# Performance work log

Measured on AMD Instinct MI355X. Metric: run time of the kernel, lower is better.

## Reference

```python
import jax, jax.numpy as jnp
import numpy as np
from jax import lax

EPS = 1e-12  # F.normalize default eps


def setup_inputs() -> dict:
    key = jax.random.key(0)
    ks = jax.random.split(key, 4)
    b, dim, h, w = 8, 192, 128, 128
    num_heads = 6
    x = jax.random.normal(ks[0], (b, dim, h, w), dtype=jnp.float32)
    y = jax.random.normal(ks[1], (b, dim, h, w), dtype=jnp.float32)
    # depthwise conv weight (groups = 3*dim): [3*dim, 1, 3, 3]
    w_dw = jax.random.normal(ks[2], (3 * dim, 1, 3, 3), dtype=jnp.float32) * 0.1
    # 1x1 projection: [dim, dim]
    w_proj = jax.random.normal(ks[3], (dim, dim), dtype=jnp.float32) * (1.0 / np.sqrt(dim))
    temperature = jnp.ones((num_heads, 1, 1), dtype=jnp.float32)
    return {"x": x, "y": y, "w_dw": w_dw, "w_proj": w_proj,
            "temperature": temperature, "num_heads": num_heads}


def _l2norm(t):
    n = jnp.sqrt(jnp.sum(t * t, axis=-1, keepdims=True))
    return t / jnp.maximum(n, EPS)


def reference(x, y, w_dw, w_proj, temperature, num_heads):
    b, c, h, w = x.shape
    qkv_in = jnp.concatenate([x, y, y], axis=1)  # [b, 3c, h, w]
    # depthwise 3x3 conv, stride 1, padding 1 (groups = 3c)
    qkv = lax.conv_general_dilated(
        qkv_in, w_dw, window_strides=(1, 1), padding=((1, 1), (1, 1)),
        dimension_numbers=("NCHW", "OIHW", "NCHW"), feature_group_count=3 * c)
    q, k, v = jnp.split(qkv, 3, axis=1)
    ch = c // num_heads
    rs = lambda t: t.reshape(b, num_heads, ch, h * w)  # b head c (h w)
    q, k, v = rs(q), rs(k), rs(v)
    q = _l2norm(q)
    k = _l2norm(k)
    # channel attention: [b, head, ch, ch]
    attn = jnp.einsum("bhcn,bhdn->bhcd", q, k) * temperature
    attn = jax.nn.softmax(attn, axis=-1)
    out = jnp.einsum("bhcd,bhdn->bhcn", attn, v).reshape(b, c, h, w)
    # 1x1 conv projection
    out = jnp.einsum("oc,bchw->bohw", w_proj, out)
    return out
```

## Files before the change

### kernel.cpp

```cpp
#include <hip/hip_runtime.h>
#include <hip/hip_bf16.h>

#define DEV __device__ __forceinline__

typedef unsigned char u8;
typedef unsigned short u16;
typedef unsigned int u32;
typedef long long i64;
typedef __attribute__((ext_vector_type(8))) short short8;
typedef __attribute__((ext_vector_type(4))) float f32x4;

DEV u16 f2bf(float f) {
  __hip_bfloat16 h = __float2bfloat16(f);
  return *(u16*)&h;
}

#define NB 8
#define NH 6
#define CTOT 192
#define HW 16384
#define VTS 34
#define LSTR 136

__global__ __launch_bounds__(256) void kconv(
    const float* __restrict__ x, const float* __restrict__ y,
    const float* __restrict__ wdw,
    u8* __restrict__ qws, u8* __restrict__ kws, u16* __restrict__ vws,
    float* __restrict__ sqq, float* __restrict__ sqk)
{
  __shared__ __align__(16) float lds[34 * LSTR];
  const int t = threadIdx.x, lane = t & 63;
  const int bx   = blockIdx.x;
  const int iskv = bx & 1;
  const int rest = bx >> 1;
  const int qtr  = rest & 3;
  const int task = rest >> 2;
  const int b  = task / 192;
  const int gc = task % 192;
  const int r0 = qtr * 32;

  const float* __restrict__ in =
      (iskv ? y : x) + (((size_t)(b * CTOT + gc)) << 14);

  float w0[9], w1[9];
  if (!iskv) {
#pragma unroll
    for (int i = 0; i < 9; ++i) w0[i] = wdw[gc * 9 + i];
  } else {
#pragma unroll
    for (int i = 0; i < 9; ++i) {
      w0[i] = wdw[(CTOT + gc) * 9 + i];
      w1[i] = wdw[(2 * CTOT + gc) * 9 + i];
    }
  }

  if (t < 68) {
    const int row = t >> 1;
    lds[row * LSTR + ((t & 1) ? 132 : 3)] = 0.f;
  }
#pragma unroll
  for (int i = 0; i < 5; ++i) {
    const int idx = i * 256 + t;
    if (idx < 1088) {
      const int row = idx >> 5, c4 = idx & 31;
      const int grow = r0 - 1 + row;
      float4 v = (grow >= 0 && grow < 128)
          ? *(const float4*)(in + grow * 128 + c4 * 4)
          : make_float4(0.f, 0.f, 0.f, 0.f);
      *(float4*)&lds[row * LSTR + 4 + c4 * 4] = v;
    }
  }
  __syncthreads();

  const int j   = t & 31;
  const int seg = t >> 5;
  const int lr0 = seg * 4;

  u8*  __restrict__ out0 =
      (iskv ? kws : qws) + (((size_t)(b * CTOT + gc)) << 14);
  u16* __restrict__ out1 = vws + (((size_t)(b * CTOT + gc)) << 14);

  float R[6][6];
#pragma unroll
  for (int i = 0; i < 6; ++i) {
    const int base = (lr0 + i) * LSTR + 4 * j;
    const float4 a0 = *(const float4*)&lds[base];
    const float4 m  = *(const float4*)&lds[base + 4];
    const float4 a2 = *(const float4*)&lds[base + 8];
    R[i][0] = a0.w; R[i][1] = m.x; R[i][2] = m.y;
    R[i][3] = m.z;  R[i][4] = m.w; R[i][5] = a2.x;
  }

  float ssum = 0.f;

#pragma unroll
  for (int k = 0; k < 4; ++k) {
    const int r = r0 + lr0 + k;

    {
      float o0 = 0.f, o1 = 0.f, o2 = 0.f, o3 = 0.f;
#pragma unroll
      for (int dr = 0; dr < 3; ++dr) {
        const float* d = R[k + dr];
        o0 = fmaf(w0[dr * 3 + 0], d[0], o0); o0 = fmaf(w0[dr * 3 + 1], d[1], o0); o0 = fmaf(w0[dr * 3 + 2], d[2], o0);
        o1 = fmaf(w0[dr * 3 + 0], d[1], o1); o1 = fmaf(w0[dr * 3 + 1], d[2], o1); o1 = fmaf(w0[dr * 3 + 2], d[3], o1);
        o2 = fmaf(w0[dr * 3 + 0], d[2], o2); o2 = fmaf(w0[dr * 3 + 1], d[3], o2); o2 = fmaf(w0[dr * 3 + 2], d[4], o2);
        o3 = fmaf(w0[dr * 3 + 0], d[3], o3); o3 = fmaf(w0[dr * 3 + 1], d[4], o3); o3 = fmaf(w0[dr * 3 + 2], d[5], o3);
      }
      ssum = fmaf(o0, o0, ssum); ssum = fmaf(o1, o1, ssum);
      ssum = fmaf(o2, o2, ssum); ssum = fmaf(o3, o3, ssum);
      u32 p = (u32)__builtin_amdgcn_cvt_pk_fp8_f32(o0, o1, 0, false);
      p = (u32)__builtin_amdgcn_cvt_pk_fp8_f32(o2, o3, (int)p, true);
      *(u32*)(out0 + r * 128 + 4 * j) = p;
    }
    if (iskv) {
      float o0 = 0.f, o1 = 0.f, o2 = 0.f, o3 = 0.f;
#pragma unroll
      for (int dr = 0; dr < 3; ++dr) {
        const float* d = R[k + dr];
        o0 = fmaf(w1[dr * 3 + 0], d[0], o0); o0 = fmaf(w1[dr * 3 + 1], d[1], o0); o0 = fmaf(w1[dr * 3 + 2], d[2], o0);
        o1 = fmaf(w1[dr * 3 + 0], d[1], o1); o1 = fmaf(w1[dr * 3 + 1], d[2], o1); o1 = fmaf(w1[dr * 3 + 2], d[3], o1);
        o2 = fmaf(w1[dr * 3 + 0], d[2], o2); o2 = fmaf(w1[dr * 3 + 1], d[3], o2); o2 = fmaf(w1[dr * 3 + 2], d[4], o2);
        o3 = fmaf(w1[dr * 3 + 0], d[3], o3); o3 = fmaf(w1[dr * 3 + 1], d[4], o3); o3 = fmaf(w1[dr * 3 + 2], d[5], o3);
      }
      const u32 p01 = ((u32)f2bf(o1) << 16) | (u32)f2bf(o0);
      const u32 p23 = ((u32)f2bf(o3) << 16) | (u32)f2bf(o2);
      *(uint2*)(out1 + r * 128 + 4 * j) = make_uint2(p01, p23);
    }
  }

  ssum += __shfl_xor(ssum, 1);
  ssum += __shfl_xor(ssum, 2);
  ssum += __shfl_xor(ssum, 4);
  ssum += __shfl_xor(ssum, 8);
  ssum += __shfl_xor(ssum, 16);
  ssum += __shfl_xor(ssum, 32);
  if (lane == 0)
    atomicAdd((iskv ? sqk : sqq) + b * CTOT + gc, ssum);
}

__global__ __launch_bounds__(256) void k2a_gram(
    const u8* __restrict__ qws, const u8* __restrict__ kws,
    float* __restrict__ gram)
{
  const int t = threadIdx.x, l = t & 63, w = t >> 6;
  const int bh = blockIdx.x >> 4, tile = blockIdx.x & 15;
  const int p0 = tile * 1024 + w * 256;
  const u8* qb = qws + (((size_t)bh) << 19);
  const u8* kb = kws + (((size_t)bh) << 19);
  const int row = l & 15;
  const int kq  = (l >> 4) * 8;

  f32x4 acc[2][2] = {};

  for (int ks = 0; ks < 8; ++ks) {
    const int p = p0 + ks * 32 + kq;
    i64 av[2], bv[2];
#pragma unroll
    for (int tc = 0; tc < 2; ++tc) {
      av[tc] = *(const i64*)(qb + (((size_t)(tc * 16 + row)) << 14) + p);
      bv[tc] = *(const i64*)(kb + (((size_t)(tc * 16 + row)) << 14) + p);
    }
#pragma unroll
    for (int tc = 0; tc < 2; ++tc)
#pragma unroll
      for (int td = 0; td < 2; ++td)
        acc[tc][td] = __builtin_amdgcn_mfma_f32_16x16x32_fp8_fp8(av[tc], bv[td], acc[tc][td], 0, 0, 0);
  }

#pragma unroll
  for (int tc = 0; tc < 2; ++tc)
#pragma unroll
    for (int td = 0; td < 2; ++td)
#pragma unroll
      for (int rr = 0; rr < 4; ++rr) {
        int c = tc * 16 + (l >> 4) * 4 + rr;
        int d = td * 16 + row;
        atomicAdd(gram + (size_t)bh * 1024 + c * 32 + d, acc[tc][td][rr]);
      }
}

__global__ __launch_bounds__(256) void k2b_w2(
    const float* __restrict__ gram, const float* __restrict__ sqq,
    const float* __restrict__ sqk, const float* __restrict__ wp,
    const float* __restrict__ temp, u16* __restrict__ W2)
{
  __shared__ float Ls[32][33];
  __shared__ float As[32][33];
  __shared__ float wl[192 * 32];
  __shared__ float nq[32], nk[32];
  const int t = threadIdx.x;
  const int bh = blockIdx.x, b = bh / 6, h = bh % 6;
  const float tmp = temp[h];
  if (t < 32) nq[t] = fmaxf(sqrtf(sqq[b * CTOT + h * 32 + t]), 1e-12f);
  else if (t < 64) nk[t - 32] = fmaxf(sqrtf(sqk[b * CTOT + h * 32 + t - 32]), 1e-12f);
  __syncthreads();
#pragma unroll
  for (int i = 0; i < 4; ++i) {
    int idx = i * 256 + t, c = idx >> 5, d = idx & 31;
    Ls[c][d] = gram[(size_t)bh * 1024 + idx] / (nq[c] * nk[d]) * tmp;
  }
  __syncthreads();
  if (t < 32) {
    float m = -1e30f;
#pragma unroll
    for (int d = 0; d < 32; ++d) m = fmaxf(m, Ls[t][d]);
    float s = 0.f;
#pragma unroll
    for (int d = 0; d < 32; ++d) s += expf(Ls[t][d] - m);
    float inv = 1.0f / s;
#pragma unroll
    for (int d = 0; d < 32; ++d) As[t][d] = expf(Ls[t][d] - m) * inv;
  }
  for (int i = 0; i < 24; ++i) {
    int idx = i * 256 + t, o = idx >> 5, c = idx & 31;
    wl[idx] = wp[o * 192 + h * 32 + c];
  }
  __syncthreads();
  for (int i = 0; i < 24; ++i) {
    int idx = i * 256 + t, o = idx >> 5, d = idx & 31;
    float a = 0.f;
#pragma unroll
    for (int c = 0; c < 32; ++c) a = fmaf(wl[o * 32 + c], As[c][d], a);
    W2[((size_t)(b * 192 + o)) * 192 + h * 32 + d] = f2bf(a);
  }
}

__global__ __launch_bounds__(256) void k3_gemm(
    const u16* __restrict__ W2, const u16* __restrict__ vnat,
    float* __restrict__ out)
{
  __shared__ __align__(16) u16 b_tile[128 * VTS];
  __shared__ __align__(16) float cout[32 * 132];
  const int t = threadIdx.x, l = t & 63, w = t >> 6;
  const int bx = blockIdx.x;
  const int b  = bx >> 7, nb = bx & 127;
  const int arow = l & 15;
  const int kq8  = (l >> 4) * 8;
  const u16* w2b = W2 + (size_t)b * 192 * 192;
  const u16* vb  = vnat + ((size_t)b * CTOT) * HW;
  const int n0 = nb * 128;

  f32x4 acc[12][2] = {};

  for (int ks = 0; ks < 6; ++ks) {
    if (ks > 0) __syncthreads();
#pragma unroll
    for (int r2 = 0; r2 < 2; ++r2) {
      const int ch   = (t >> 4) + r2 * 16;
      const int nseg = (t & 15) * 8;
      short8 vv = *(const short8*)(vb + (size_t)(ks * 32 + ch) * HW + n0 + nseg);
#pragma unroll
      for (int j = 0; j < 8; ++j) b_tile[(nseg + j) * VTS + ch] = (u16)vv[j];
    }
    __syncthreads();

    short8 bf[2];
#pragma unroll
    for (int nt = 0; nt < 2; ++nt)
      bf[nt] = *(const short8*)&b_tile[(w * 32 + nt * 16 + arow) * VTS + kq8];
#pragma unroll
    for (int ot = 0; ot < 12; ++ot) {
      short8 af = *(const short8*)(w2b + (size_t)(ot * 16 + arow) * 192 + ks * 32 + kq8);
#pragma unroll
      for (int nt = 0; nt < 2; ++nt)
        acc[ot][nt] = __builtin_amdgcn_mfma_f32_16x16x32_bf16(af, bf[nt], acc[ot][nt], 0, 0, 0);
    }
  }

  float* __restrict__ ob = out + ((size_t)b * 192) * 16384;
#pragma unroll
  for (int og = 0; og < 6; ++og) {
    __syncthreads();
#pragma unroll
    for (int oi = 0; oi < 2; ++oi) {
#pragma unroll
      for (int nt = 0; nt < 2; ++nt)
#pragma unroll
        for (int rr = 0; rr < 4; ++rr) {
          const int o_l = oi * 16 + (l >> 4) * 4 + rr;
          const int n_l = w * 32 + nt * 16 + (l & 15);
          cout[o_l * 132 + n_l] = acc[og * 2 + oi][nt][rr];
        }
    }
    __syncthreads();
    const int o_l = t >> 3;
    const int o   = og * 32 + o_l;
#pragma unroll
    for (int c = 0; c < 4; ++c) {
      const int n = (t & 7) * 4 + c * 32;
      float4 v4;
      v4.x = cout[o_l * 132 + n + 0];
      v4.y = cout[o_l * 132 + n + 1];
      v4.z = cout[o_l * 132 + n + 2];
      v4.w = cout[o_l * 132 + n + 3];
      *(float4*)(ob + (size_t)o * 16384 + n0 + n) = v4;
    }
  }
}

extern "C" void kernel_launch(void* const* d_in, const int* in_sizes, int n_in,
                              void* d_out, int out_size, void* d_ws, size_t ws_size,
                              hipStream_t stream)
{
  const float* x    = (const float*)d_in[0];
  const float* y    = (const float*)d_in[1];
  const float* wdw  = (const float*)d_in[2];
  const float* wp   = (const float*)d_in[3];
  const float* temp = (const float*)d_in[4];

  char* ws = (char*)d_ws;
  const size_t QK8 = (size_t)NB * CTOT * HW;
  const size_t VBF = (size_t)NB * CTOT * HW * 2;
  u8*    qws  = (u8*)(ws);
  u8*    kws  = (u8*)(ws + QK8);
  u16*   vws  = (u16*)(ws + 2 * QK8);
  char*  meta = ws + 2 * QK8 + VBF;
  float* gram = (float*)(meta);
  float* sqq  = (float*)(meta + 196608);
  float* sqk  = (float*)(meta + 196608 + 6144);
  u16*   W2   = (u16*)(meta + 196608 + 12288);
  float* out  = (float*)d_out;

  hipMemsetAsync(meta, 0, 208896, stream);
  kconv<<<12288, 256, 0, stream>>>(x, y, wdw, qws, kws, vws, sqq, sqk);
  k2a_gram<<<768, 256, 0, stream>>>(qws, kws, gram);
  k2b_w2<<<48, 256, 0, stream>>>(gram, sqq, sqk, wp, temp, W2);
  k3_gemm<<<1024, 256, 0, stream>>>(W2, vws, out);
}
```

Before: 167.8 us.

## Double-buffer conv input via direct global-to-LDS loads, merge x/y blocks

Rewrites the depthwise conv kernel so each block handles half an image for both x and y channels, staging 16-row tiles into double-buffered LDS with global_load_lds while the previous tile is computed. Grid shrinks from 12288 to 3072 blocks, and the q, k and v convs plus both sum-of-squares reductions happen in one block. Out-of-range halo rows read from the zeroed gram buffer instead of branching, and column halos are handled by neighbour-index clamping. This aims to hide load latency and cut per-block overhead, at the cost of more LDS per block and reliance on the gram buffer being zero when kconv runs.

```diff
diff --git a/kernel.cpp b/kernel.cpp
--- a/kernel.cpp
+++ b/kernel.cpp
@@ -20,123 +20,135 @@
 #define CTOT 192
 #define HW 16384
 #define VTS 34
-#define LSTR 136
+#define SLAB 2304
+
+DEV void gload_lds(const float* src, float* dst) {
+  __builtin_amdgcn_global_load_lds(
+      (const __attribute__((address_space(1))) void*)src,
+      (__attribute__((address_space(3))) void*)dst, 16, 0, 0);
+}
 
 __global__ __launch_bounds__(256) void kconv(
     const float* __restrict__ x, const float* __restrict__ y,
-    const float* __restrict__ wdw,
+    const float* __restrict__ wdw, const float* __restrict__ zp,
     u8* __restrict__ qws, u8* __restrict__ kws, u16* __restrict__ vws,
     float* __restrict__ sqq, float* __restrict__ sqk)
 {
-  __shared__ __align__(16) float lds[34 * LSTR];
-  const int t = threadIdx.x, lane = t & 63;
+  __shared__ __align__(16) float bufX[2][SLAB];
+  __shared__ __align__(16) float bufY[2][SLAB];
+  const int t = threadIdx.x, lane = t & 63, w = t >> 6;
   const int bx   = blockIdx.x;
-  const int iskv = bx & 1;
-  const int rest = bx >> 1;
-  const int qtr  = rest & 3;
-  const int task = rest >> 2;
+  const int half = bx & 1;
+  const int task = bx >> 1;
   const int b  = task / 192;
   const int gc = task % 192;
-  const int r0 = qtr * 32;
-
-  const float* __restrict__ in =
-      (iskv ? y : x) + (((size_t)(b * CTOT + gc)) << 14);
-
-  float w0[9], w1[9];
-  if (!iskv) {
-#pragma unroll
-    for (int i = 0; i < 9; ++i) w0[i] = wdw[gc * 9 + i];
-  } else {
-#pragma unroll
-    for (int i = 0; i < 9; ++i) {
-      w0[i] = wdw[(CTOT + gc) * 9 + i];
-      w1[i] = wdw[(2 * CTOT + gc) * 9 + i];
-    }
-  }
-
-  if (t < 68) {
-    const int row = t >> 1;
-    lds[row * LSTR + ((t & 1) ? 132 : 3)] = 0.f;
-  }
-#pragma unroll
-  for (int i = 0; i < 5; ++i) {
-    const int idx = i * 256 + t;
-    if (idx < 1088) {
-      const int row = idx >> 5, c4 = idx & 31;
-      const int grow = r0 - 1 + row;
-      float4 v = (grow >= 0 && grow < 128)
-          ? *(const float4*)(in + grow * 128 + c4 * 4)
-          : make_float4(0.f, 0.f, 0.f, 0.f);
-      *(float4*)&lds[row * LSTR + 4 + c4 * 4] = v;
-    }
-  }
-  __syncthreads();
+  const int r0 = half * 64;
+
+  const float* __restrict__ inx = x + (((size_t)(b * CTOT + gc)) << 14);
+  const float* __restrict__ iny = y + (((size_t)(b * CTOT + gc)) << 14);
+
+  float wq[9], wk[9], wv[9];
+#pragma unroll
+  for (int i = 0; i < 9; ++i) {
+    wq[i] = wdw[gc * 9 + i];
+    wk[i] = wdw[(CTOT + gc) * 9 + i];
+    wv[i] = wdw[(2 * CTOT + gc) * 9 + i];
+  }
+
+  #define STAGE(bb, tt) { \
+      const int tr0s = r0 + (tt) * 16; \
+      const int px = (lane & 31) * 4; \
+      for (int l = w; l < 9; l += 4) { \
+        const int srow = tr0s - 1 + 2 * l + (lane >> 5); \
+        const bool ok = (srow >= 0) && (srow < 128); \
+        const float* sx = ok ? (inx + srow * 128 + px) : (zp + px); \
+        const float* sy = ok ? (iny + srow * 128 + px) : (zp + px); \
+        gload_lds(sx, &bufX[bb][l * 256]); \
+        gload_lds(sy, &bufY[bb][l * 256]); \
+      } }
 
   const int j   = t & 31;
   const int seg = t >> 5;
-  const int lr0 = seg * 4;
-
-  u8*  __restrict__ out0 =
-      (iskv ? kws : qws) + (((size_t)(b * CTOT + gc)) << 14);
-  u16* __restrict__ out1 = vws + (((size_t)(b * CTOT + gc)) << 14);
-
-  float R[6][6];
-#pragma unroll
-  for (int i = 0; i < 6; ++i) {
-    const int base = (lr0 + i) * LSTR + 4 * j;
-    const float4 a0 = *(const float4*)&lds[base];
-    const float4 m  = *(const float4*)&lds[base + 4];
-    const float4 a2 = *(const float4*)&lds[base + 8];
-    R[i][0] = a0.w; R[i][1] = m.x; R[i][2] = m.y;
-    R[i][3] = m.z;  R[i][4] = m.w; R[i][5] = a2.x;
-  }
-
-  float ssum = 0.f;
-
-#pragma unroll
-  for (int k = 0; k < 4; ++k) {
-    const int r = r0 + lr0 + k;
-
-    {
-      float o0 = 0.f, o1 = 0.f, o2 = 0.f, o3 = 0.f;
-#pragma unroll
-      for (int dr = 0; dr < 3; ++dr) {
-        const float* d = R[k + dr];
-        o0 = fmaf(w0[dr * 3 + 0], d[0], o0); o0 = fmaf(w0[dr * 3 + 1], d[1], o0); o0 = fmaf(w0[dr * 3 + 2], d[2], o0);
-        o1 = fmaf(w0[dr * 3 + 0], d[1], o1); o1 = fmaf(w0[dr * 3 + 1], d[2], o1); o1 = fmaf(w0[dr * 3 + 2], d[3], o1);
-        o2 = fmaf(w0[dr * 3 + 0], d[2], o2); o2 = fmaf(w0[dr * 3 + 1], d[3], o2); o2 = fmaf(w0[dr * 3 + 2], d[4], o2);
-        o3 = fmaf(w0[dr * 3 + 0], d[3], o3); o3 = fmaf(w0[dr * 3 + 1], d[4], o3); o3 = fmaf(w0[dr * 3 + 2], d[5], o3);
-      }
-      ssum = fmaf(o0, o0, ssum); ssum = fmaf(o1, o1, ssum);
-      ssum = fmaf(o2, o2, ssum); ssum = fmaf(o3, o3, ssum);
+
+  u8*  __restrict__ qout = qws + (((size_t)(b * CTOT + gc)) << 14);
+  u8*  __restrict__ kout = kws + (((size_t)(b * CTOT + gc)) << 14);
+  u16* __restrict__ vout = vws + (((size_t)(b * CTOT + gc)) << 14);
+
+  float ssq = 0.f, ssk = 0.f;
+
+  #define RDROW(buf, ri, d) { \
+      const float4 A = *(const float4*)&(buf)[(ri) * 128 + (j ? 4 * j - 4 : 0)]; \
+      const float4 M = *(const float4*)&(buf)[(ri) * 128 + 4 * j]; \
+      const float4 B = *(const float4*)&(buf)[(ri) * 128 + (j < 31 ? 4 * j + 4 : 124)]; \
+      d[0] = j ? A.w : 0.f; \
+      d[1] = M.x; d[2] = M.y; d[3] = M.z; d[4] = M.w; \
+      d[5] = (j < 31) ? B.x : 0.f; }
+
+  #define CONV4(Rw, wgt, k0, o0, o1, o2, o3) { \
+      o0 = o1 = o2 = o3 = 0.f; \
+      _Pragma("unroll") \
+      for (int dr = 0; dr < 3; ++dr) { \
+        const float* d = Rw[(k0) + dr]; \
+        o0 = fmaf(wgt[dr * 3 + 0], d[0], o0); o0 = fmaf(wgt[dr * 3 + 1], d[1], o0); o0 = fmaf(wgt[dr * 3 + 2], d[2], o0); \
+        o1 = fmaf(wgt[dr * 3 + 0], d[1], o1); o1 = fmaf(wgt[dr * 3 + 1], d[2], o1); o1 = fmaf(wgt[dr * 3 + 2], d[3], o1); \
+        o2 = fmaf(wgt[dr * 3 + 0], d[2], o2); o2 = fmaf(wgt[dr * 3 + 1], d[3], o2); o2 = fmaf(wgt[dr * 3 + 2], d[4], o2); \
+        o3 = fmaf(wgt[dr * 3 + 0], d[3], o3); o3 = fmaf(wgt[dr * 3 + 1], d[4], o3); o3 = fmaf(wgt[dr * 3 + 2], d[5], o3); \
+      } }
+
+  STAGE(0, 0);
+  __syncthreads();
+
+#pragma unroll
+  for (int tt = 0; tt < 4; ++tt) {
+    if (tt < 3) STAGE((tt + 1) & 1, tt + 1);
+
+    const int bb  = tt & 1;
+    const int tr0 = r0 + tt * 16;
+
+    float RX[4][6], RY[4][6];
+#pragma unroll
+    for (int i = 0; i < 4; ++i) {
+      RDROW(bufX[bb], seg * 2 + i, RX[i]);
+      RDROW(bufY[bb], seg * 2 + i, RY[i]);
+    }
+
+#pragma unroll
+    for (int k = 0; k < 2; ++k) {
+      const int r = tr0 + seg * 2 + k;
+      float o0, o1, o2, o3;
+      CONV4(RX, wq, k, o0, o1, o2, o3);
+      ssq = fmaf(o0, o0, ssq); ssq = fmaf(o1, o1, ssq);
+      ssq = fmaf(o2, o2, ssq); ssq = fmaf(o3, o3, ssq);
       u32 p = (u32)__builtin_amdgcn_cvt_pk_fp8_f32(o0, o1, 0, false);
       p = (u32)__builtin_amdgcn_cvt_pk_fp8_f32(o2, o3, (int)p, true);
-      *(u32*)(out0 + r * 128 + 4 * j) = p;
-    }
-    if (iskv) {
-      float o0 = 0.f, o1 = 0.f, o2 = 0.f, o3 = 0.f;
-#pragma unroll
-      for (int dr = 0; dr < 3; ++dr) {
-        const float* d = R[k + dr];
-        o0 = fmaf(w1[dr * 3 + 0], d[0], o0); o0 = fmaf(w1[dr * 3 + 1], d[1], o0); o0 = fmaf(w1[dr * 3 + 2], d[2], o0);
-        o1 = fmaf(w1[dr * 3 + 0], d[1], o1); o1 = fmaf(w1[dr * 3 + 1], d[2], o1); o1 = fmaf(w1[dr * 3 + 2], d[3], o1);
-        o2 = fmaf(w1[dr * 3 + 0], d[2], o2); o2 = fmaf(w1[dr * 3 + 1], d[3], o2); o2 = fmaf(w1[dr * 3 + 2], d[4], o2);
-        o3 = fmaf(w1[dr * 3 + 0], d[3], o3); o3 = fmaf(w1[dr * 3 + 1], d[4], o3); o3 = fmaf(w1[dr * 3 + 2], d[5], o3);
-      }
+      *(u32*)(qout + r * 128 + 4 * j) = p;
+      CONV4(RY, wk, k, o0, o1, o2, o3);
+      ssk = fmaf(o0, o0, ssk); ssk = fmaf(o1, o1, ssk);
+      ssk = fmaf(o2, o2, ssk); ssk = fmaf(o3, o3, ssk);
+      p = (u32)__builtin_amdgcn_cvt_pk_fp8_f32(o0, o1, 0, false);
+      p = (u32)__builtin_amdgcn_cvt_pk_fp8_f32(o2, o3, (int)p, true);
+      *(u32*)(kout + r * 128 + 4 * j) = p;
+      CONV4(RY, wv, k, o0, o1, o2, o3);
       const u32 p01 = ((u32)f2bf(o1) << 16) | (u32)f2bf(o0);
       const u32 p23 = ((u32)f2bf(o3) << 16) | (u32)f2bf(o2);
-      *(uint2*)(out1 + r * 128 + 4 * j) = make_uint2(p01, p23);
-    }
-  }
-
-  ssum += __shfl_xor(ssum, 1);
-  ssum += __shfl_xor(ssum, 2);
-  ssum += __shfl_xor(ssum, 4);
-  ssum += __shfl_xor(ssum, 8);
-  ssum += __shfl_xor(ssum, 16);
-  ssum += __shfl_xor(ssum, 32);
-  if (lane == 0)
-    atomicAdd((iskv ? sqk : sqq) + b * CTOT + gc, ssum);
+      *(uint2*)(vout + r * 128 + 4 * j) = make_uint2(p01, p23);
+    }
+    __syncthreads();
+  }
+  #undef STAGE
+  #undef RDROW
+  #undef CONV4
+
+  ssq += __shfl_xor(ssq, 1);  ssk += __shfl_xor(ssk, 1);
+  ssq += __shfl_xor(ssq, 2);  ssk += __shfl_xor(ssk, 2);
+  ssq += __shfl_xor(ssq, 4);  ssk += __shfl_xor(ssk, 4);
+  ssq += __shfl_xor(ssq, 8);  ssk += __shfl_xor(ssk, 8);
+  ssq += __shfl_xor(ssq, 16); ssk += __shfl_xor(ssk, 16);
+  ssq += __shfl_xor(ssq, 32); ssk += __shfl_xor(ssk, 32);
+  if (lane == 0) {
+    atomicAdd(sqq + b * CTOT + gc, ssq);
+    atomicAdd(sqk + b * CTOT + gc, ssk);
+  }
 }
 
 __global__ __launch_bounds__(256) void k2a_gram(
@@ -323,7 +335,7 @@
   float* out  = (float*)d_out;
 
   hipMemsetAsync(meta, 0, 208896, stream);
-  kconv<<<12288, 256, 0, stream>>>(x, y, wdw, qws, kws, vws, sqq, sqk);
+  kconv<<<3072, 256, 0, stream>>>(x, y, wdw, gram, qws, kws, vws, sqq, sqk);
   k2a_gram<<<768, 256, 0, stream>>>(qws, kws, gram);
   k2b_w2<<<48, 256, 0, stream>>>(gram, sqq, sqk, wp, temp, W2);
   k3_gemm<<<1024, 256, 0, stream>>>(W2, vws, out);
```

Measured after the change: 154.2 us (median of 2 runs). 8.1% less time.
